# Optimization experiments

Measured on AMD Instinct MI355X. Metric: run time of the kernel, lower is better.

## Reference

```python
import jax, jax.numpy as jnp
import numpy as np

B, SQ, SK, D, H = 8, 1024, 1024, 768, 12
HD = D // H  # 64


def setup_inputs() -> dict:
    key = jax.random.key(0)
    ks = jax.random.split(key, 6)
    s = 0.02
    return {
        "hidden_states": jax.random.normal(ks[0], (B, SQ, D), jnp.float32),
        "context": jax.random.normal(ks[1], (B, SK, D), jnp.float32),
        "attention_mask": jnp.zeros((B, 1, 1, SK), jnp.float32),
        "Wq": jax.random.normal(ks[2], (D, D), jnp.float32) * s,
        "bq": jnp.zeros((D,), jnp.float32),
        "Wk": jax.random.normal(ks[3], (D, D), jnp.float32) * s,
        "bk": jnp.zeros((D,), jnp.float32),
        "Wv": jax.random.normal(ks[4], (D, D), jnp.float32) * s,
        "bv": jnp.zeros((D,), jnp.float32),
    }


def _split_heads(x):
    # [B, S, D] -> [B, H, S, HD]
    b, s, _ = x.shape
    return x.reshape(b, s, H, HD).transpose(0, 2, 1, 3)


def reference(hidden_states, context, attention_mask, Wq, bq, Wk, bk, Wv, bv):
    q = _split_heads(hidden_states @ Wq + bq)   # [B,H,SQ,HD]
    k = _split_heads(context @ Wk + bk)         # [B,H,SK,HD]
    v = _split_heads(context @ Wv + bv)         # [B,H,SK,HD]
    scores = jnp.einsum("bhqd,bhkd->bhqk", q, k) / jnp.sqrt(jnp.float32(HD))
    scores = scores + attention_mask            # broadcast [B,1,1,SK]
    probs = jax.nn.softmax(scores, axis=-1)     # dropout p=0 -> identity
    ctx = jnp.einsum("bhqk,bhkd->bhqd", probs, v)
    return ctx.transpose(0, 2, 1, 3).reshape(hidden_states.shape[0], -1, H * HD)
```

## Files before the change

### kernel.cpp

```cpp
#include <hip/hip_runtime.h>
#include <hip/hip_bf16.h>
#include <cstdint>

#define B_  8
#define SQ_ 1024
#define SK_ 1024
#define D_  768
#define H_  12
#define HD_ 64

typedef __attribute__((ext_vector_type(8))) short s16x8;
typedef __attribute__((ext_vector_type(4))) float f32x4;

__device__ __forceinline__ float bf2f(ushort u) {
    union { uint32_t i; float f; } v; v.i = ((uint32_t)u) << 16; return v.f;
}
__device__ __forceinline__ ushort f2bf(float f) {
    union { float f; uint32_t i; } v; v.f = f;
    uint32_t x = v.i;
    return (ushort)((x + 0x7fffu + ((x >> 16) & 1u)) >> 16);
}

__global__ void convX(const float4* __restrict__ src, ushort* __restrict__ dst, int n4) {
    int i = blockIdx.x * blockDim.x + threadIdx.x;
    int stride = gridDim.x * blockDim.x;
    for (; i < n4; i += stride) {
        float4 v = src[i];
        ushort4 o = { f2bf(v.x), f2bf(v.y), f2bf(v.z), f2bf(v.w) };
        *reinterpret_cast<ushort4*>(dst + (size_t)i * 4) = o;
    }
}

__global__ void convWT(const float* __restrict__ W, ushort* __restrict__ WT) {
    __shared__ float t[32][33];
    int k0 = blockIdx.x * 32, n0 = blockIdx.y * 32;
    int tx = threadIdx.x & 31, ty = threadIdx.x >> 5;
#pragma unroll
    for (int rr = 0; rr < 4; ++rr)
        t[ty + 8 * rr][tx] = W[(size_t)(k0 + ty + 8 * rr) * D_ + n0 + tx];
    __syncthreads();
#pragma unroll
    for (int rr = 0; rr < 4; ++rr)
        WT[(size_t)(n0 + ty + 8 * rr) * D_ + k0 + tx] = f2bf(t[tx][ty + 8 * rr]);
}

#define GL16(g, l)                                                                     \
    __builtin_amdgcn_global_load_lds((const __attribute__((address_space(1))) void*)(g), \
                                     (__attribute__((address_space(3))) void*)(l), 16, 0, 0)

__global__ __launch_bounds__(256) void gemm_qkv(
    const ushort* __restrict__ hb, const ushort* __restrict__ cb,
    const ushort* __restrict__ wqt, const ushort* __restrict__ wkt, const ushort* __restrict__ wvt,
    const float* __restrict__ bq, const float* __restrict__ bk, const float* __restrict__ bv,
    ushort* __restrict__ qout, ushort* __restrict__ kout, ushort* __restrict__ vtout)
{
    const int z = blockIdx.z;
    const ushort* A    = (z == 0) ? hb : cb;
    const ushort* Wt   = (z == 0) ? wqt : (z == 1) ? wkt : wvt;
    const float*  bias = (z == 0) ? bq  : (z == 1) ? bk  : bv;

    __shared__ ushort As[128 * 32];
    __shared__ ushort Bs[128 * 32];

    const int tid = threadIdx.x;
    const int w = tid >> 6, l = tid & 63;
    const int g = l >> 4, c = l & 15;
    const int wr = w >> 1, wc = w & 1;
    const int m0 = blockIdx.x * 128;
    const int n0 = blockIdx.y * 128;

    f32x4 acc[4][4];
#pragma unroll
    for (int mi = 0; mi < 4; ++mi)
#pragma unroll
        for (int ni = 0; ni < 4; ++ni) acc[mi][ni] = (f32x4){0.f, 0.f, 0.f, 0.f};

    for (int kt = 0; kt < D_ / 32; ++kt) {
        __syncthreads();
#pragma unroll
        for (int j = 0; j < 2; ++j) {
            int cc = (j * 4 + w) * 64 + l;
            int row = cc >> 2, c8 = cc & 3;
            const ushort* ga = A  + (size_t)(m0 + row) * D_ + kt * 32 + c8 * 8;
            GL16(ga, (char*)As + (size_t)(j * 4 + w) * 1024);
            const ushort* gb = Wt + (size_t)(n0 + row) * D_ + kt * 32 + c8 * 8;
            GL16(gb, (char*)Bs + (size_t)(j * 4 + w) * 1024);
        }
        __syncthreads();

        s16x8 af[4], bfr[4];
#pragma unroll
        for (int mi = 0; mi < 4; ++mi)
            af[mi] = *(const s16x8*)&As[(wr * 64 + mi * 16 + c) * 32 + g * 8];
#pragma unroll
        for (int ni = 0; ni < 4; ++ni)
            bfr[ni] = *(const s16x8*)&Bs[(wc * 64 + ni * 16 + c) * 32 + g * 8];
#pragma unroll
        for (int mi = 0; mi < 4; ++mi)
#pragma unroll
            for (int ni = 0; ni < 4; ++ni)
                acc[mi][ni] = __builtin_amdgcn_mfma_f32_16x16x32_bf16(af[mi], bfr[ni], acc[mi][ni], 0, 0, 0);
    }

    if (z < 2) {
        ushort* Out = (z == 0) ? qout : kout;
#pragma unroll
        for (int ni = 0; ni < 4; ++ni) {
            int ncol = n0 + wc * 64 + ni * 16 + c;
            float bv_ = bias[ncol];
#pragma unroll
            for (int mi = 0; mi < 4; ++mi) {
#pragma unroll
                for (int r = 0; r < 4; ++r) {
                    int mrow = m0 + wr * 64 + mi * 16 + 4 * g + r;
                    Out[(size_t)mrow * D_ + ncol] = f2bf(acc[mi][ni][r] + bv_);
                }
            }
        }
    } else {
#pragma unroll
        for (int ni = 0; ni < 4; ++ni) {
            int ncol = n0 + wc * 64 + ni * 16 + c;
            float bv_ = bias[ncol];
            int hh = ncol >> 6, dd = ncol & 63;
#pragma unroll
            for (int mi = 0; mi < 4; ++mi) {
                int mrow = m0 + wr * 64 + mi * 16 + 4 * g;
                int bb = mrow >> 10, ss = mrow & 1023;
                ushort4 pk;
                pk.x = f2bf(acc[mi][ni][0] + bv_);
                pk.y = f2bf(acc[mi][ni][1] + bv_);
                pk.z = f2bf(acc[mi][ni][2] + bv_);
                pk.w = f2bf(acc[mi][ni][3] + bv_);
                *reinterpret_cast<ushort4*>(vtout + (size_t)((bb * H_ + hh) * HD_ + dd) * SK_ + ss) = pk;
            }
        }
    }
}

__global__ __launch_bounds__(256) void attn(
    const ushort* __restrict__ Qb, const ushort* __restrict__ Kb, const ushort* __restrict__ VT,
    const float* __restrict__ amask, float* __restrict__ out)
{
    __shared__ ushort Ks[64 * 64];
    __shared__ ushort Vs[64 * 64];
    __shared__ ushort Ps[4][16 * 64];

    const int tid = threadIdx.x;
    const int w = tid >> 6, l = tid & 63;
    const int g = l >> 4, c = l & 15;
    const int q0 = blockIdx.x * 64;
    const int h  = blockIdx.y;
    const int b  = blockIdx.z;

    s16x8 qf[2];
#pragma unroll
    for (int kk = 0; kk < 2; ++kk) {
        const ushort* gq = Qb + (size_t)(b * SQ_ + q0 + w * 16 + c) * D_ + h * HD_ + kk * 32 + g * 8;
        s16x8 v = *(const s16x8*)gq;
#pragma unroll
        for (int i = 0; i < 8; ++i) v[i] = (short)f2bf(bf2f((ushort)v[i]) * 0.125f);
        qf[kk] = v;
    }

    f32x4 o[4];
#pragma unroll
    for (int nn = 0; nn < 4; ++nn) o[nn] = (f32x4){0.f, 0.f, 0.f, 0.f};
    float m_run[4], l_run[4];
#pragma unroll
    for (int r = 0; r < 4; ++r) { m_run[r] = -INFINITY; l_run[r] = 0.f; }

    const float L2E = 1.44269504f;

    for (int t = 0; t < SK_ / 64; ++t) {
        const int kv0 = t * 64;
        __syncthreads();
#pragma unroll
        for (int j = 0; j < 2; ++j) {
            int cc = j * 256 + tid;
            int row = cc >> 3, c8 = cc & 7;
            int ldsb = row * 128 + ((c8 * 16) ^ ((row & 7) << 4));
            uint4 kv_ = *(const uint4*)(Kb + (size_t)(b * SK_ + kv0 + row) * D_ + h * HD_ + c8 * 8);
            *(uint4*)((char*)Ks + ldsb) = kv_;
            uint4 vv_ = *(const uint4*)(VT + (size_t)((b * H_ + h) * HD_ + row) * SK_ + kv0 + c8 * 8);
            *(uint4*)((char*)Vs + ldsb) = vv_;
        }
        __syncthreads();

        float sv[4][4];
#pragma unroll
        for (int n = 0; n < 4; ++n) {
            f32x4 s = (f32x4){0.f, 0.f, 0.f, 0.f};
#pragma unroll
            for (int kk = 0; kk < 2; ++kk) {
                const s16x8 bf_ = *(const s16x8*)((const char*)Ks + (16 * n + c) * 128 +
                                                  ((kk * 64 + g * 16) ^ ((c & 7) << 4)));
                s = __builtin_amdgcn_mfma_f32_16x16x32_bf16(qf[kk], bf_, s, 0, 0, 0);
            }
            float mv = amask[b * SK_ + kv0 + 16 * n + c];
#pragma unroll
            for (int r = 0; r < 4; ++r) sv[n][r] = s[r] + mv;
        }

        float rmax[4], alpha[4], rsum[4];
#pragma unroll
        for (int r = 0; r < 4; ++r) {
            rmax[r] = fmaxf(fmaxf(sv[0][r], sv[1][r]), fmaxf(sv[2][r], sv[3][r]));
            rmax[r] = fmaxf(rmax[r], __shfl_xor(rmax[r], 1));
            rmax[r] = fmaxf(rmax[r], __shfl_xor(rmax[r], 2));
            rmax[r] = fmaxf(rmax[r], __shfl_xor(rmax[r], 4));
            rmax[r] = fmaxf(rmax[r], __shfl_xor(rmax[r], 8));
        }
#pragma unroll
        for (int r = 0; r < 4; ++r) {
            float mn = fmaxf(m_run[r], rmax[r]);
            alpha[r] = exp2f((m_run[r] - mn) * L2E);
            m_run[r] = mn;
            rsum[r] = 0.f;
        }
#pragma unroll
        for (int n = 0; n < 4; ++n)
#pragma unroll
            for (int r = 0; r < 4; ++r) {
                float p = exp2f((sv[n][r] - m_run[r]) * L2E);
                sv[n][r] = p;
                rsum[r] += p;
            }
#pragma unroll
        for (int r = 0; r < 4; ++r) {
            rsum[r] += __shfl_xor(rsum[r], 1);
            rsum[r] += __shfl_xor(rsum[r], 2);
            rsum[r] += __shfl_xor(rsum[r], 4);
            rsum[r] += __shfl_xor(rsum[r], 8);
            l_run[r] = l_run[r] * alpha[r] + rsum[r];
        }
#pragma unroll
        for (int nn = 0; nn < 4; ++nn)
#pragma unroll
            for (int r = 0; r < 4; ++r) o[nn][r] *= alpha[r];

#pragma unroll
        for (int n = 0; n < 4; ++n)
#pragma unroll
            for (int r = 0; r < 4; ++r) {
                int row = 4 * g + r;
                *(ushort*)((char*)&Ps[w][0] + row * 128 +
                           (((16 * n + c) * 2) ^ ((row & 7) << 4))) = f2bf(sv[n][r]);
            }
        s16x8 pa[2];
#pragma unroll
        for (int kk = 0; kk < 2; ++kk)
            pa[kk] = *(const s16x8*)((const char*)&Ps[w][0] + c * 128 +
                                     ((kk * 64 + g * 16) ^ ((c & 7) << 4)));
#pragma unroll
        for (int nn = 0; nn < 4; ++nn) {
#pragma unroll
            for (int kk = 0; kk < 2; ++kk) {
                const s16x8 bv_ = *(const s16x8*)((const char*)Vs + (16 * nn + c) * 128 +
                                                  ((kk * 64 + g * 16) ^ ((c & 7) << 4)));
                o[nn] = __builtin_amdgcn_mfma_f32_16x16x32_bf16(pa[kk], bv_, o[nn], 0, 0, 0);
            }
        }
    }

    float inv[4];
#pragma unroll
    for (int r = 0; r < 4; ++r) inv[r] = 1.f / l_run[r];
#pragma unroll
    for (int nn = 0; nn < 4; ++nn)
#pragma unroll
        for (int r = 0; r < 4; ++r)
            out[(size_t)(b * SQ_ + q0 + w * 16 + 4 * g + r) * D_ + h * HD_ + 16 * nn + c] =
                o[nn][r] * inv[r];
}

extern "C" void kernel_launch(void* const* d_in, const int* in_sizes, int n_in,
                              void* d_out, int out_size, void* d_ws, size_t ws_size,
                              hipStream_t stream) {
    (void)in_sizes; (void)n_in; (void)out_size; (void)ws_size;
    const float* hidden  = (const float*)d_in[0];
    const float* context = (const float*)d_in[1];
    const float* amask   = (const float*)d_in[2];
    const float* Wq = (const float*)d_in[3];
    const float* bq = (const float*)d_in[4];
    const float* Wk = (const float*)d_in[5];
    const float* bk = (const float*)d_in[6];
    const float* Wv = (const float*)d_in[7];
    const float* bv = (const float*)d_in[8];
    float* out = (float*)d_out;

    char* ws = (char*)d_ws;
    ushort* hb  = (ushort*)(ws);
    ushort* cb  = (ushort*)(ws + 12582912);
    ushort* wqt = (ushort*)(ws + 25165824);
    ushort* wkt = (ushort*)(ws + 26345472);
    ushort* wvt = (ushort*)(ws + 27525120);
    ushort* qb  = (ushort*)(ws + 28704768);
    ushort* kb  = (ushort*)(ws + 41287680);
    ushort* vt  = (ushort*)(ws + 53870592);

    int n4 = (B_ * SQ_ * D_) / 4;
    convX<<<2048, 256, 0, stream>>>((const float4*)hidden, hb, n4);
    convX<<<2048, 256, 0, stream>>>((const float4*)context, cb, n4);
    dim3 gw(24, 24);
    convWT<<<gw, 256, 0, stream>>>(Wq, wqt);
    convWT<<<gw, 256, 0, stream>>>(Wk, wkt);
    convWT<<<gw, 256, 0, stream>>>(Wv, wvt);
    gemm_qkv<<<dim3(64, 6, 3), 256, 0, stream>>>(hb, cb, wqt, wkt, wvt, bq, bk, bv, qb, kb, vt);
    attn<<<dim3(16, 12, 8), 256, 0, stream>>>(qb, kb, vt, amask, out);
}
```

Before: 262.6 us.

## Use lazy max rescaling and deferred row-sum reduction in flash attention softmax

The online softmax now skips the cross-lane max reduction and the rescaling of the output accumulator unless some row's tile max exceeds the running max by more than a threshold of 8. This is checked wave-wide with __all. Each lane keeps its own partial row sum, and the cross-lane shuffle reduction happens once at the end instead of on every KV tile. The bf16 conversion also switches to the library __float2bfloat16. This removes many shuffles and exp/multiply operations per tile, at the cost of unnormalised exponentials that can grow up to e^8 before rescaling, which is tolerable in fp32 but a little riskier when P is rounded to bf16.

```diff
diff --git a/kernel.cpp b/kernel.cpp
--- a/kernel.cpp
+++ b/kernel.cpp
@@ -16,9 +16,8 @@
     union { uint32_t i; float f; } v; v.i = ((uint32_t)u) << 16; return v.f;
 }
 __device__ __forceinline__ ushort f2bf(float f) {
-    union { float f; uint32_t i; } v; v.f = f;
-    uint32_t x = v.i;
-    return (ushort)((x + 0x7fffu + ((x >> 16) & 1u)) >> 16);
+    __hip_bfloat16 h = __float2bfloat16(f);
+    union { __hip_bfloat16 h; ushort u; } v; v.h = h; return v.u;
 }
 
 __global__ void convX(const float4* __restrict__ src, ushort* __restrict__ dst, int n4) {
@@ -166,9 +165,9 @@
     f32x4 o[4];
 #pragma unroll
     for (int nn = 0; nn < 4; ++nn) o[nn] = (f32x4){0.f, 0.f, 0.f, 0.f};
-    float m_run[4], l_run[4];
-#pragma unroll
-    for (int r = 0; r < 4; ++r) { m_run[r] = -INFINITY; l_run[r] = 0.f; }
+    float m_run[4], ps[4];
+#pragma unroll
+    for (int r = 0; r < 4; ++r) { m_run[r] = -INFINITY; ps[r] = 0.f; }
 
     const float L2E = 1.44269504f;
 
@@ -202,21 +201,31 @@
             for (int r = 0; r < 4; ++r) sv[n][r] = s[r] + mv;
         }
 
-        float rmax[4], alpha[4], rsum[4];
-#pragma unroll
-        for (int r = 0; r < 4; ++r) {
-            rmax[r] = fmaxf(fmaxf(sv[0][r], sv[1][r]), fmaxf(sv[2][r], sv[3][r]));
-            rmax[r] = fmaxf(rmax[r], __shfl_xor(rmax[r], 1));
-            rmax[r] = fmaxf(rmax[r], __shfl_xor(rmax[r], 2));
-            rmax[r] = fmaxf(rmax[r], __shfl_xor(rmax[r], 4));
-            rmax[r] = fmaxf(rmax[r], __shfl_xor(rmax[r], 8));
-        }
-#pragma unroll
-        for (int r = 0; r < 4; ++r) {
-            float mn = fmaxf(m_run[r], rmax[r]);
-            alpha[r] = exp2f((m_run[r] - mn) * L2E);
-            m_run[r] = mn;
-            rsum[r] = 0.f;
+        float pmax[4];
+#pragma unroll
+        for (int r = 0; r < 4; ++r)
+            pmax[r] = fmaxf(fmaxf(sv[0][r], sv[1][r]), fmaxf(sv[2][r], sv[3][r]));
+        int ok = 1;
+#pragma unroll
+        for (int r = 0; r < 4; ++r) ok &= (pmax[r] <= m_run[r] + 8.f);
+        if (!__all(ok)) {
+            float alpha[4];
+#pragma unroll
+            for (int r = 0; r < 4; ++r) {
+                float m_ = pmax[r];
+                m_ = fmaxf(m_, __shfl_xor(m_, 1));
+                m_ = fmaxf(m_, __shfl_xor(m_, 2));
+                m_ = fmaxf(m_, __shfl_xor(m_, 4));
+                m_ = fmaxf(m_, __shfl_xor(m_, 8));
+                float mn = fmaxf(m_run[r], m_);
+                alpha[r] = exp2f((m_run[r] - mn) * L2E);
+                m_run[r] = mn;
+                ps[r] *= alpha[r];
+            }
+#pragma unroll
+            for (int nn = 0; nn < 4; ++nn)
+#pragma unroll
+                for (int r = 0; r < 4; ++r) o[nn][r] *= alpha[r];
         }
 #pragma unroll
         for (int n = 0; n < 4; ++n)
@@ -224,20 +233,8 @@
             for (int r = 0; r < 4; ++r) {
                 float p = exp2f((sv[n][r] - m_run[r]) * L2E);
                 sv[n][r] = p;
-                rsum[r] += p;
-            }
-#pragma unroll
-        for (int r = 0; r < 4; ++r) {
-            rsum[r] += __shfl_xor(rsum[r], 1);
-            rsum[r] += __shfl_xor(rsum[r], 2);
-            rsum[r] += __shfl_xor(rsum[r], 4);
-            rsum[r] += __shfl_xor(rsum[r], 8);
-            l_run[r] = l_run[r] * alpha[r] + rsum[r];
-        }
-#pragma unroll
-        for (int nn = 0; nn < 4; ++nn)
-#pragma unroll
-            for (int r = 0; r < 4; ++r) o[nn][r] *= alpha[r];
+                ps[r] += p;
+            }
 
 #pragma unroll
         for (int n = 0; n < 4; ++n)
@@ -265,7 +262,14 @@
 
     float inv[4];
 #pragma unroll
-    for (int r = 0; r < 4; ++r) inv[r] = 1.f / l_run[r];
+    for (int r = 0; r < 4; ++r) {
+        float s_ = ps[r];
+        s_ += __shfl_xor(s_, 1);
+        s_ += __shfl_xor(s_, 2);
+        s_ += __shfl_xor(s_, 4);
+        s_ += __shfl_xor(s_, 8);
+        inv[r] = 1.f / s_;
+    }
 #pragma unroll
     for (int nn = 0; nn < 4; ++nn)
 #pragma unroll
```

Measured after the change: 238.1 us. 9.3% less time.
